# Kernel tuning notes

Hardware: AMD Instinct MI355X
Metric: run time of the kernel (lower is better)

The kernel has to match this reference:

```python
import jax, jax.numpy as jnp
import numpy as np

LRELU_SLOPE = 0.2
ACT_GAIN = float(np.sqrt(2.0))  # def_gain of lrelu in StyleGAN2
CLAMP = 256.0


def _affine(w, W, b):
    # StyleGAN2 FullyConnectedLayer: runtime weight gain 1/sqrt(in_features)
    return w @ W.T * (1.0 / np.sqrt(W.shape[1])) + b[None, :]


def _gather(x, fn, pad):
    # zero rows for padding faces appended at the end, then neighborhood gather
    padded = jnp.concatenate([x, jnp.zeros((pad, x.shape[1]), x.dtype)], axis=0)
    return padded[fn]  # [N, K, C]


def _mod_texture_conv(g, styles, wc, wsd, wcr):
    # g: [N, 9, I] gathered neighborhoods; styles: [B, I]
    B, I = styles.shape
    N = g.shape[0]
    F = N // B
    # position-typed 1x1 weights: [self, 4 sides, 4 corners] -> [O, I, 9]
    W = jnp.concatenate([wc[:, :, None],
                         jnp.repeat(wsd[:, :, None], 4, axis=2),
                         jnp.repeat(wcr[:, :, None], 4, axis=2)], axis=2)
    wmod = W[None] * styles[:, None, :, None]                    # [B,O,I,9] modulate
    d = jax.lax.rsqrt(jnp.sum(wmod * wmod, axis=(2, 3)) + 1e-8)  # [B,O] demodulate
    wmod = wmod * d[:, :, None, None]
    out = jnp.einsum('bfki,boik->bfok', g.reshape(B, F, 9, I), wmod)
    return out.max(axis=3).reshape(N, -1)  # MaxPool2d((1,9)) aggregation


def _smooth_upsample(x, pool_map, fn, pad):
    # replicate coarse face features to fine faces, then smooth over 9-neighborhood
    return _gather(x[pool_map], fn, pad).mean(axis=1)


def _act(x, bias):
    # clamp_gain(lrelu(x+b), act_gain*gain, 256*gain) with gain=1
    return jnp.clip(jax.nn.leaky_relu(x + bias[None, :], LRELU_SLOPE) * ACT_GAIN, -CLAMP, CLAMP)


def setup_inputs() -> dict:
    key = jax.random.key(0)
    ks = iter(jax.random.split(key, 40))
    B, Fc, Ff = 1, 32768, 131072
    IN, OUT, GEO, COL, WD = 128, 128, 32, 3, 512
    OC1 = OUT - GEO  # 96
    PAD0, PAD1 = 1024, 4096
    nk = lambda *s: jax.random.normal(next(ks), s, jnp.float32)
    ri = lambda shape, hi: jax.random.randint(next(ks), shape, 0, hi, jnp.int32).astype(jnp.int64)
    return dict(
        x=nk(B * Fc, IN - GEO), shape_feat=nk(B * Fc, GEO), img=nk(B * Fc, COL),
        ws=nk(B, 3, WD),
        fn0=ri((B * Fc, 9), B * Fc + PAD0), fn1=ri((B * Ff, 9), B * Ff + PAD1),
        pool_map0=ri((B * Ff,), B * Fc),
        pad0=PAD0, pad1=PAD1,
        affine0_w=nk(IN, WD), affine0_b=jnp.ones((IN,), jnp.float32),
        w_center0=nk(OUT, IN), w_side0=nk(OUT, IN), w_corner0=nk(OUT, IN),
        noise_strength0=nk(1) * 0.1, bias0=nk(OUT) * 0.1, noise_const0=nk(Ff),
        affine1_w=nk(OUT, WD), affine1_b=jnp.ones((OUT,), jnp.float32),
        w_center1=nk(OC1, OUT), w_side1=nk(OC1, OUT), w_corner1=nk(OC1, OUT),
        noise_strength1=nk(1) * 0.1, bias1=nk(OC1) * 0.1, noise_const1=nk(Ff),
        affine2_w=nk(OC1, WD), affine2_b=jnp.ones((OC1,), jnp.float32),
        w_rgb=nk(COL, OC1), bias_rgb=nk(COL) * 0.1,
    )


def reference(x, shape_feat, img, ws, fn0, fn1, pool_map0, pad0, pad1,
              affine0_w, affine0_b, w_center0, w_side0, w_corner0,
              noise_strength0, bias0, noise_const0,
              affine1_w, affine1_b, w_center1, w_side1, w_corner1,
              noise_strength1, bias1, noise_const1,
              affine2_w, affine2_b, w_rgb, bias_rgb):
    B = ws.shape[0]
    h = jnp.concatenate([x, shape_feat], axis=1)  # [B*Fc, IN]
    # ---- conv0: coarse-level modulated face conv, then SmoothUpsample to fine ----
    s0 = _affine(ws[:, 0], affine0_w, affine0_b)
    h = _mod_texture_conv(_gather(h, fn0, pad0), s0, w_center0, w_side0, w_corner0)
    h = _smooth_upsample(h, pool_map0, fn1, pad1)  # [B*Ff, OUT]
    h = h + jnp.tile(noise_const0[None, :], (B, 1)).reshape(-1, 1) * noise_strength0
    h = _act(h, bias0)
    # ---- conv1: fine-level modulated face conv ----
    s1 = _affine(ws[:, 1], affine1_w, affine1_b)
    h = _mod_texture_conv(_gather(h, fn1, pad1), s1, w_center1, w_side1, w_corner1)
    h = h + jnp.tile(noise_const1[None, :], (B, 1)).reshape(-1, 1) * noise_strength1
    h = _act(h, bias1)  # [B*Ff, 96]
    # ---- torgb: 1x1 modulated conv (demodulate=False), weight_gain on styles ----
    s2 = _affine(ws[:, 2], affine2_w, affine2_b) * (1.0 / np.sqrt(w_rgb.shape[1]))
    xg = _gather(h, fn1[:, :1], pad1)[:, 0]  # kernel_size^2 == 1 -> self gather
    y = jnp.einsum('bfi,oi,bi->bfo', xg.reshape(B, -1, xg.shape[1]), w_rgb, s2)
    y = jnp.clip(y.reshape(xg.shape[0], -1) + bias_rgb[None, :], -CLAMP, CLAMP)
    img_out = _smooth_upsample(img, pool_map0, fn1, pad1) + y
    return h, img_out
```

## Files before the change

kernel.cpp:

```cpp
#include <hip/hip_runtime.h>

#define FC 32768
#define FF 131072
#define LRELU_SLOPE 0.2f
#define ACT_GAIN 1.4142135623730951f
#define CLAMP_V 256.0f

typedef __bf16 bf16x8 __attribute__((ext_vector_type(8)));
typedef float f32x4 __attribute__((ext_vector_type(4)));
typedef float f32x2 __attribute__((ext_vector_type(2)));
typedef unsigned u32x4 __attribute__((ext_vector_type(4)));
typedef unsigned u32x2 __attribute__((ext_vector_type(2)));
typedef unsigned short u16x4 __attribute__((ext_vector_type(4)));

static __device__ __forceinline__ unsigned short f2bf(float f) {
    unsigned u = __float_as_uint(f);
    u += 0x7FFFu + ((u >> 16) & 1u);
    return (unsigned short)(u >> 16);
}
static __device__ __forceinline__ unsigned packbf(float a, float b) {
    return (unsigned)f2bf(a) | ((unsigned)f2bf(b) << 16);
}
static __device__ __forceinline__ float bf2f(unsigned short u) {
    return __uint_as_float(((unsigned)u) << 16);
}
static __device__ __forceinline__ float actf(float v) {
    v = (v < 0.f) ? v * LRELU_SLOPE : v;
    v *= ACT_GAIN;
    return fminf(fmaxf(v, -CLAMP_V), CLAMP_V);
}
static __device__ __forceinline__ int xcd_swz(int bid, int nwg) {
    return (bid & 7) * (nwg >> 3) + (bid >> 3);
}

__global__ void k_prep2(const float* __restrict__ wsvec,
                        const float* __restrict__ a0w, const float* __restrict__ a0b,
                        const float* __restrict__ a1w, const float* __restrict__ a1b,
                        const float* __restrict__ a2w, const float* __restrict__ a2b,
                        float* __restrict__ s0, float* __restrict__ s1, float* __restrict__ s2,
                        unsigned* __restrict__ zrow)
{
    int lane = threadIdx.x & 63;
    int t = blockIdx.x * 4 + (threadIdx.x >> 6);
    if (t >= 352) {
        if (t == 352) zrow[lane] = 0u;
        return;
    }
    int level, o;
    const float *W, *bptr; float* out;
    if (t < 128)       { level = 0; o = t;       W = a0w; bptr = a0b; out = s0; }
    else if (t < 256)  { level = 1; o = t - 128; W = a1w; bptr = a1b; out = s1; }
    else               { level = 2; o = t - 256; W = a2w; bptr = a2b; out = s2; }
    const float* wrow = wsvec + level * 512;
    const float* Wr = W + (size_t)o * 512;
    f32x4 wa = *(const f32x4*)(wrow + lane * 8);
    f32x4 wb = *(const f32x4*)(wrow + lane * 8 + 4);
    f32x4 va = *(const f32x4*)(Wr + lane * 8);
    f32x4 vb = *(const f32x4*)(Wr + lane * 8 + 4);
    float acc = wa.x * va.x + wa.y * va.y + wa.z * va.z + wa.w * va.w
              + wb.x * vb.x + wb.y * vb.y + wb.z * vb.z + wb.w * vb.w;
    #pragma unroll
    for (int off = 32; off; off >>= 1) acc += __shfl_down(acc, off, 64);
    if (lane == 0) {
        float v = acc * 0.04419417382415922f + bptr[o];
        if (level == 2) v *= 0.10206207261596577f;
        out[o] = v;
    }
}

__global__ void k_misc(const float* __restrict__ x, const float* __restrict__ sf,
                       u16x4* __restrict__ xcat,
                       const int* __restrict__ fn1, const int* __restrict__ pmap,
                       int* __restrict__ cidx)
{
    int b = blockIdx.x;
    if (b < FC * 32 / 256) {
        int gid = b * 256 + threadIdx.x;
        int f = gid >> 5;
        int c4 = (gid & 31) * 4;
        f32x4 v;
        if (c4 < 96) v = *(const f32x4*)(x + (size_t)f * 96 + c4);
        else         v = *(const f32x4*)(sf + (size_t)f * 32 + (c4 - 96));
        u16x4 o;
        o.x = f2bf(v.x); o.y = f2bf(v.y); o.z = f2bf(v.z); o.w = f2bf(v.w);
        xcat[gid] = o;
    } else {
        int gid = (b - FC * 32 / 256) * 256 + threadIdx.x;
        int g = fn1[gid];
        cidx[gid] = ((unsigned)g < FF) ? pmap[g] : -1;
    }
}

__global__ void k_wmod(const float* __restrict__ wc0, const float* __restrict__ wsd0,
                       const float* __restrict__ wcr0, const float* __restrict__ s0,
                       unsigned short* __restrict__ wm0,
                       const float* __restrict__ wc1, const float* __restrict__ wsd1,
                       const float* __restrict__ wcr1, const float* __restrict__ s1,
                       unsigned short* __restrict__ wm1,
                       const float* __restrict__ wrgb, const float* __restrict__ s2,
                       float* __restrict__ wrgbmod)
{
    int b = blockIdx.x;
    int i = threadIdx.x;
    if (b == 224) {
        for (int t = i; t < 288; t += 128) {
            int c = t / 96, k = t % 96;
            wrgbmod[c * 96 + k] = wrgb[c * 96 + k] * s2[k];
        }
        return;
    }
    const float *wc, *wsd, *wcr, *s; unsigned short* out; int o, O;
    if (b < 128) { wc = wc0; wsd = wsd0; wcr = wcr0; s = s0; out = wm0; o = b; O = 128; }
    else         { wc = wc1; wsd = wsd1; wcr = wcr1; s = s1; out = wm1; o = b - 128; O = 96; }
    float sv = s[i];
    float pc = wc[o * 128 + i] * sv;
    float ps = wsd[o * 128 + i] * sv;
    float pr = wcr[o * 128 + i] * sv;
    float part = pc * pc + 4.f * ps * ps + 4.f * pr * pr;
    __shared__ float red[2];
    #pragma unroll
    for (int off = 32; off; off >>= 1) part += __shfl_down(part, off, 64);
    if ((threadIdx.x & 63) == 0) red[threadIdx.x >> 6] = part;
    __syncthreads();
    float d = rsqrtf(red[0] + red[1] + 1e-8f);
    out[(0 * O + o) * 128 + i] = f2bf(pc * d);
    out[(1 * O + o) * 128 + i] = f2bf(ps * d);
    out[(2 * O + o) * 128 + i] = f2bf(pr * d);
}

__launch_bounds__(256, 2)
__global__ void k_fgemm0(const unsigned short* __restrict__ xcat,
                         const unsigned short* __restrict__ wm,
                         const int* __restrict__ fn0,
                         const unsigned* __restrict__ zrow,
                         unsigned* __restrict__ hc0)
{
    __shared__ char ldsw[65536];
    int bid = xcd_swz(blockIdx.x, gridDim.x);
    int lane = threadIdx.x & 63;
    int w = threadIdx.x >> 6;
    int fgrp = w >> 1;
    int mtb = (w & 1) * 4;
    int fbase = (bid * 2 + fgrp) * 16;
    int quad = lane >> 4, l15 = lane & 15;
    int face = fbase + l15;
    const char* hb = (const char*)xcat;
    const char* wb = (const char*)wm;

    #pragma unroll
    for (int i0 = 0; i0 < 16; ++i0) {
        int i = i0 * 256 + threadIdx.x;
        u32x4 v = *(const u32x4*)(wb + 32768 + (size_t)i * 16);
        int r = i >> 4, c = i & 15;
        *(u32x4*)(ldsw + r * 256 + ((c ^ (r & 7)) * 16)) = v;
    }
    __syncthreads();

    int id[9];
    #pragma unroll
    for (int j = 0; j < 9; ++j) id[j] = fn0[(size_t)face * 9 + j];

    f32x4 ymax[4];
    #pragma unroll
    for (int mi = 0; mi < 4; ++mi)
        #pragma unroll
        for (int r = 0; r < 4; ++r) ymax[mi][r] = -3.0e38f;

    int xr = l15 & 7;

    #pragma unroll
    for (int j = 0; j < 9; ++j) {
        const int t = (j == 0) ? 0 : ((j < 5) ? 1 : 2);
        const char* src = ((unsigned)id[j] < FC) ? (hb + (size_t)id[j] * 256) : (const char*)zrow;
        bf16x8 bfr[4];
        #pragma unroll
        for (int s = 0; s < 4; ++s)
            bfr[s] = *(const bf16x8*)(src + s * 64 + quad * 16);
        f32x4 acc[4];
        #pragma unroll
        for (int mi = 0; mi < 4; ++mi)
            #pragma unroll
            for (int r = 0; r < 4; ++r) acc[mi][r] = 0.f;
        #pragma unroll
        for (int s = 0; s < 4; ++s) {
            #pragma unroll
            for (int mi = 0; mi < 4; ++mi) {
                bf16x8 afr;
                if (t == 0)
                    afr = *(const bf16x8*)(wb + (size_t)((((mtb + mi) * 16 + l15) * 128 + s * 32 + quad * 8) * 2));
                else
                    afr = *(const bf16x8*)(ldsw + ((t - 1) * 128 + (mtb + mi) * 16 + l15) * 256
                                                + (((s * 4 + quad) ^ xr) * 16));
                acc[mi] = __builtin_amdgcn_mfma_f32_16x16x32_bf16(afr, bfr[s], acc[mi], 0, 0, 0);
            }
        }
        #pragma unroll
        for (int mi = 0; mi < 4; ++mi)
            #pragma unroll
            for (int r = 0; r < 4; ++r)
                ymax[mi][r] = fmaxf(ymax[mi][r], acc[mi][r]);
    }

    #pragma unroll
    for (int mi = 0; mi < 4; ++mi) {
        u32x2 v;
        v.x = packbf(ymax[mi][0], ymax[mi][1]);
        v.y = packbf(ymax[mi][2], ymax[mi][3]);
        *(u32x2*)(hc0 + (size_t)face * 64 + (mtb + mi) * 8 + quad * 2) = v;
    }
}

__global__ void k_upsample(const unsigned* __restrict__ hc, const int* __restrict__ cidx,
                           const float* __restrict__ nco0,
                           const float* __restrict__ ns0p, const float* __restrict__ bias0,
                           unsigned* __restrict__ h1u, const unsigned* __restrict__ zrow)
{
    int bid = xcd_swz(blockIdx.x, gridDim.x);
    int gid = bid * 256 + threadIdx.x;
    int f = gid >> 4;
    int c = gid & 15;
    int id[9];
    #pragma unroll
    for (int j = 0; j < 9; ++j) id[j] = cidx[f * 9 + j];
    u32x4 v[9];
    #pragma unroll
    for (int j = 0; j < 9; ++j) {
        const unsigned* p = (id[j] >= 0) ? (hc + (size_t)id[j] * 64) : zrow;
        v[j] = *(const u32x4*)(p + c * 4);
    }
    float nz = nco0[f] * ns0p[0];
    f32x4 b0 = *(const f32x4*)(bias0 + c * 8);
    f32x4 b1 = *(const f32x4*)(bias0 + c * 8 + 4);
    const float inv9 = 1.f / 9.f;
    u32x4 out;
    #pragma unroll
    for (int k = 0; k < 4; ++k) {
        float a0 = 0.f, a1 = 0.f;
        #pragma unroll
        for (int j = 0; j < 9; ++j) {
            a0 += bf2f((unsigned short)v[j][k]);
            a1 += bf2f((unsigned short)(v[j][k] >> 16));
        }
        float bb0 = (k < 2) ? ((k == 0) ? b0.x : b0.z) : ((k == 2) ? b1.x : b1.z);
        float bb1 = (k < 2) ? ((k == 0) ? b0.y : b0.w) : ((k == 2) ? b1.y : b1.w);
        a0 = actf(a0 * inv9 + nz + bb0);
        a1 = actf(a1 * inv9 + nz + bb1);
        out[k] = packbf(a0, a1);
    }
    *(u32x4*)(h1u + (size_t)f * 64 + c * 4) = out;
}

__launch_bounds__(256, 2)
__global__ void k_fgemm1(const unsigned short* __restrict__ h1,
                         const unsigned short* __restrict__ wm,
                         const int* __restrict__ fn1,
                         const unsigned* __restrict__ zrow,
                         const float* __restrict__ nco1, const float* __restrict__ ns1p,
                         const float* __restrict__ bias1, const float* __restrict__ wrgbmod,
                         float* __restrict__ hout, f32x4* __restrict__ rgb3)
{
    __shared__ char ldsw[49152];
    int bid = xcd_swz(blockIdx.x, gridDim.x);
    int lane = threadIdx.x & 63;
    int w = threadIdx.x >> 6;
    int fbase = (bid * 4 + w) * 16;
    int quad = lane >> 4, l15 = lane & 15;
    int face = fbase + l15;
    const char* hb = (const char*)h1;
    const char* wb = (const char*)wm;

    #pragma unroll
    for (int i0 = 0; i0 < 12; ++i0) {
        int i = i0 * 256 + threadIdx.x;
        u32x4 v = *(const u32x4*)(wb + 24576 + (size_t)i * 16);
        int r = i >> 4, c = i & 15;
        *(u32x4*)(ldsw + r * 256 + ((c ^ (r & 7)) * 16)) = v;
    }
    __syncthreads();

    int id[9];
    #pragma unroll
    for (int j = 0; j < 9; ++j) id[j] = fn1[(size_t)face * 9 + j];

    f32x4 ymax[6];
    #pragma unroll
    for (int mt = 0; mt < 6; ++mt)
        #pragma unroll
        for (int r = 0; r < 4; ++r) ymax[mt][r] = -3.0e38f;

    int xr = l15 & 7;

    #pragma unroll
    for (int j = 0; j < 9; ++j) {
        const int t = (j == 0) ? 0 : ((j < 5) ? 1 : 2);
        const char* src = ((unsigned)id[j] < FF) ? (hb + (size_t)id[j] * 256) : (const char*)zrow;
        bf16x8 bfr[4];
        #pragma unroll
        for (int s = 0; s < 4; ++s)
            bfr[s] = *(const bf16x8*)(src + s * 64 + quad * 16);
        f32x4 acc[6];
        #pragma unroll
        for (int mt = 0; mt < 6; ++mt)
            #pragma unroll
            for (int r = 0; r < 4; ++r) acc[mt][r] = 0.f;
        #pragma unroll
        for (int s = 0; s < 4; ++s) {
            #pragma unroll
            for (int mt = 0; mt < 6; ++mt) {
                bf16x8 afr;
                if (t == 0)
                    afr = *(const bf16x8*)(wb + (size_t)(((mt * 16 + l15) * 128 + s * 32 + quad * 8) * 2));
                else
                    afr = *(const bf16x8*)(ldsw + ((t - 1) * 96 + mt * 16 + l15) * 256
                                                + (((s * 4 + quad) ^ xr) * 16));
                acc[mt] = __builtin_amdgcn_mfma_f32_16x16x32_bf16(afr, bfr[s], acc[mt], 0, 0, 0);
            }
        }
        #pragma unroll
        for (int mt = 0; mt < 6; ++mt)
            #pragma unroll
            for (int r = 0; r < 4; ++r)
                ymax[mt][r] = fmaxf(ymax[mt][r], acc[mt][r]);
    }

    float ns1 = ns1p[0];
    float nz = nco1[face] * ns1;
    float p0 = 0.f, p1 = 0.f, p2 = 0.f;
    #pragma unroll
    for (int mt = 0; mt < 6; ++mt) {
        f32x4 bv = *(const f32x4*)(bias1 + mt * 16 + quad * 4);
        f32x4 hv;
        #pragma unroll
        for (int r = 0; r < 4; ++r) hv[r] = actf(ymax[mt][r] + nz + bv[r]);
        __builtin_nontemporal_store(hv, (f32x4*)(hout + (size_t)face * 96 + mt * 16 + quad * 4));
        f32x4 w0 = *(const f32x4*)(wrgbmod + mt * 16 + quad * 4);
        f32x4 w1 = *(const f32x4*)(wrgbmod + 96 + mt * 16 + quad * 4);
        f32x4 w2 = *(const f32x4*)(wrgbmod + 192 + mt * 16 + quad * 4);
        p0 += hv.x * w0.x + hv.y * w0.y + hv.z * w0.z + hv.w * w0.w;
        p1 += hv.x * w1.x + hv.y * w1.y + hv.z * w1.z + hv.w * w1.w;
        p2 += hv.x * w2.x + hv.y * w2.y + hv.z * w2.z + hv.w * w2.w;
    }
    p0 += __shfl_xor(p0, 16, 64); p0 += __shfl_xor(p0, 32, 64);
    p1 += __shfl_xor(p1, 16, 64); p1 += __shfl_xor(p1, 32, 64);
    p2 += __shfl_xor(p2, 16, 64); p2 += __shfl_xor(p2, 32, 64);
    if (quad == 0) {
        f32x4 o; o.x = p0; o.y = p1; o.z = p2; o.w = 0.f;
        rgb3[face] = o;
    }
}

__global__ void k_torgb2(const f32x4* __restrict__ rgb3, const int* __restrict__ fn1,
                         const int* __restrict__ cidx, const float* __restrict__ img,
                         const float* __restrict__ brgb, float* __restrict__ imgout)
{
    int f = blockIdx.x * 256 + threadIdx.x;
    int g0 = fn1[(size_t)f * 9];
    float y0 = 0.f, y1 = 0.f, y2 = 0.f;
    if ((unsigned)g0 < FF) {
        f32x4 y = rgb3[g0];
        y0 = y.x; y1 = y.y; y2 = y.z;
    }
    y0 = fminf(fmaxf(y0 + brgb[0], -CLAMP_V), CLAMP_V);
    y1 = fminf(fmaxf(y1 + brgb[1], -CLAMP_V), CLAMP_V);
    y2 = fminf(fmaxf(y2 + brgb[2], -CLAMP_V), CLAMP_V);
    float i0 = 0.f, i1 = 0.f, i2 = 0.f;
    #pragma unroll
    for (int j = 0; j < 9; ++j) {
        int id = cidx[f * 9 + j];
        if (id >= 0) {
            const float* ir = img + (size_t)id * 3;
            i0 += ir[0]; i1 += ir[1]; i2 += ir[2];
        }
    }
    const float inv9 = 1.f / 9.f;
    imgout[(size_t)f * 3 + 0] = i0 * inv9 + y0;
    imgout[(size_t)f * 3 + 1] = i1 * inv9 + y1;
    imgout[(size_t)f * 3 + 2] = i2 * inv9 + y2;
}

extern "C" void kernel_launch(void* const* d_in, const int* in_sizes, int n_in,
                              void* d_out, int out_size, void* d_ws, size_t ws_size,
                              hipStream_t stream) {
    const float* x     = (const float*)d_in[0];
    const float* sfeat = (const float*)d_in[1];
    const float* img   = (const float*)d_in[2];
    const float* wsv   = (const float*)d_in[3];
    const int* fn0     = (const int*)d_in[4];
    const int* fn1     = (const int*)d_in[5];
    const int* pmap    = (const int*)d_in[6];
    const float* a0w   = (const float*)d_in[9];
    const float* a0b   = (const float*)d_in[10];
    const float* wc0   = (const float*)d_in[11];
    const float* wsd0  = (const float*)d_in[12];
    const float* wcr0  = (const float*)d_in[13];
    const float* ns0   = (const float*)d_in[14];
    const float* bias0 = (const float*)d_in[15];
    const float* nco0  = (const float*)d_in[16];
    const float* a1w   = (const float*)d_in[17];
    const float* a1b   = (const float*)d_in[18];
    const float* wc1   = (const float*)d_in[19];
    const float* wsd1  = (const float*)d_in[20];
    const float* wcr1  = (const float*)d_in[21];
    const float* ns1   = (const float*)d_in[22];
    const float* bias1 = (const float*)d_in[23];
    const float* nco1  = (const float*)d_in[24];
    const float* a2w   = (const float*)d_in[25];
    const float* a2b   = (const float*)d_in[26];
    const float* wrgb  = (const float*)d_in[27];
    const float* brgb  = (const float*)d_in[28];

    char* wsb = (char*)d_ws;
    float* s0            = (float*)(wsb + 0);
    float* s1            = (float*)(wsb + 512);
    float* s2            = (float*)(wsb + 1024);
    float* wrgbmod       = (float*)(wsb + 1536);
    unsigned* zrow       = (unsigned*)(wsb + 4096);
    unsigned short* wm0  = (unsigned short*)(wsb + 8192);
    unsigned short* wm1  = (unsigned short*)(wsb + 8192 + 98304);
    unsigned short* xcat = (unsigned short*)(wsb + 262144);
    unsigned* hc0        = (unsigned*)(wsb + 33816576);
    unsigned short* h1   = (unsigned short*)(wsb + 42205184);
    int* cidx            = (int*)(wsb + 75759616);
    f32x4* rgb3          = (f32x4*)(wsb + 155975680);

    float* out_h   = (float*)d_out;
    float* out_img = out_h + (size_t)FF * 96;

    k_misc<<<FC * 32 / 256 + FF * 9 / 256, 256, 0, stream>>>(x, sfeat, (u16x4*)xcat, fn1, pmap, cidx);
    k_prep2<<<89, 256, 0, stream>>>(wsv, a0w, a0b, a1w, a1b, a2w, a2b, s0, s1, s2, zrow);
    k_wmod<<<225, 128, 0, stream>>>(wc0, wsd0, wcr0, s0, wm0,
                                    wc1, wsd1, wcr1, s1, wm1, wrgb, s2, wrgbmod);
    k_fgemm0<<<FC / 32, 256, 0, stream>>>(xcat, wm0, fn0, zrow, hc0);
    k_upsample<<<FF * 16 / 256, 256, 0, stream>>>(hc0, cidx, nco0, ns0, bias0, (unsigned*)h1, zrow);
    k_fgemm1<<<FF / 64, 256, 0, stream>>>(h1, wm1, fn1, zrow, nco1, ns1, bias1, wrgbmod,
                                          out_h, rgb3);
    k_torgb2<<<FF / 256, 256, 0, stream>>>(rgb3, fn1, cidx, img, brgb, out_img);
}
```

Measured before the change: 287.6 us.

## Double-buffer neighbor gathers and split fgemm1 output channels across wave pairs

```diff
diff --git a/kernel.cpp b/kernel.cpp
--- a/kernel.cpp
+++ b/kernel.cpp
@@ -8,7 +8,6 @@
 
 typedef __bf16 bf16x8 __attribute__((ext_vector_type(8)));
 typedef float f32x4 __attribute__((ext_vector_type(4)));
-typedef float f32x2 __attribute__((ext_vector_type(2)));
 typedef unsigned u32x4 __attribute__((ext_vector_type(4)));
 typedef unsigned u32x2 __attribute__((ext_vector_type(2)));
 typedef unsigned short u16x4 __attribute__((ext_vector_type(4)));
@@ -168,14 +167,25 @@
 
     int xr = l15 & 7;
 
-    #pragma unroll
-    for (int j = 0; j < 9; ++j) {
-        const int t = (j == 0) ? 0 : ((j < 5) ? 1 : 2);
-        const char* src = ((unsigned)id[j] < FC) ? (hb + (size_t)id[j] * 256) : (const char*)zrow;
-        bf16x8 bfr[4];
-        #pragma unroll
-        for (int s = 0; s < 4; ++s)
-            bfr[s] = *(const bf16x8*)(src + s * 64 + quad * 16);
+    bf16x8 b0[4], b1[4];
+    {
+        const char* src = ((unsigned)id[1] < FC) ? (hb + (size_t)id[1] * 256) : (const char*)zrow;
+        #pragma unroll
+        for (int s = 0; s < 4; ++s) b0[s] = *(const bf16x8*)(src + s * 64 + quad * 16);
+    }
+
+    #pragma unroll
+    for (int jj = 1; jj <= 8; ++jj) {
+        const int t = (jj < 5) ? 1 : 2;
+        const int nj = (jj < 8) ? (jj + 1) : 0;
+        {
+            const char* src = ((unsigned)id[nj] < FC) ? (hb + (size_t)id[nj] * 256) : (const char*)zrow;
+            #pragma unroll
+            for (int s = 0; s < 4; ++s) {
+                bf16x8 v = *(const bf16x8*)(src + s * 64 + quad * 16);
+                if (jj & 1) b1[s] = v; else b0[s] = v;
+            }
+        }
         f32x4 acc[4];
         #pragma unroll
         for (int mi = 0; mi < 4; ++mi)
@@ -183,15 +193,33 @@
             for (int r = 0; r < 4; ++r) acc[mi][r] = 0.f;
         #pragma unroll
         for (int s = 0; s < 4; ++s) {
+            bf16x8 cur = (jj & 1) ? b0[s] : b1[s];
             #pragma unroll
             for (int mi = 0; mi < 4; ++mi) {
-                bf16x8 afr;
-                if (t == 0)
-                    afr = *(const bf16x8*)(wb + (size_t)((((mtb + mi) * 16 + l15) * 128 + s * 32 + quad * 8) * 2));
-                else
-                    afr = *(const bf16x8*)(ldsw + ((t - 1) * 128 + (mtb + mi) * 16 + l15) * 256
-                                                + (((s * 4 + quad) ^ xr) * 16));
-                acc[mi] = __builtin_amdgcn_mfma_f32_16x16x32_bf16(afr, bfr[s], acc[mi], 0, 0, 0);
+                bf16x8 afr = *(const bf16x8*)(ldsw + ((t - 1) * 128 + (mtb + mi) * 16 + l15) * 256
+                                                   + (((s * 4 + quad) ^ xr) * 16));
+                acc[mi] = __builtin_amdgcn_mfma_f32_16x16x32_bf16(afr, cur, acc[mi], 0, 0, 0);
+            }
+        }
+        #pragma unroll
+        for (int mi = 0; mi < 4; ++mi)
+            #pragma unroll
+            for (int r = 0; r < 4; ++r)
+                ymax[mi][r] = fmaxf(ymax[mi][r], acc[mi][r]);
+    }
+
+    {
+        f32x4 acc[4];
+        #pragma unroll
+        for (int mi = 0; mi < 4; ++mi)
+            #pragma unroll
+            for (int r = 0; r < 4; ++r) acc[mi][r] = 0.f;
+        #pragma unroll
+        for (int s = 0; s < 4; ++s) {
+            #pragma unroll
+            for (int mi = 0; mi < 4; ++mi) {
+                bf16x8 afr = *(const bf16x8*)(wb + (size_t)((((mtb + mi) * 16 + l15) * 128 + s * 32 + quad * 8) * 2));
+                acc[mi] = __builtin_amdgcn_mfma_f32_16x16x32_bf16(afr, b0[s], acc[mi], 0, 0, 0);
             }
         }
         #pragma unroll
@@ -260,10 +288,14 @@
                          float* __restrict__ hout, f32x4* __restrict__ rgb3)
 {
     __shared__ char ldsw[49152];
+    __shared__ float rgx[2][16][4];
     int bid = xcd_swz(blockIdx.x, gridDim.x);
     int lane = threadIdx.x & 63;
     int w = threadIdx.x >> 6;
-    int fbase = (bid * 4 + w) * 16;
+    int fgrp = w >> 1;
+    int chh = w & 1;
+    int mtb = chh * 3;
+    int fbase = (bid * 2 + fgrp) * 16;
     int quad = lane >> 4, l15 = lane & 15;
     int face = fbase + l15;
     const char* hb = (const char*)h1;
@@ -282,56 +314,86 @@
     #pragma unroll
     for (int j = 0; j < 9; ++j) id[j] = fn1[(size_t)face * 9 + j];
 
-    f32x4 ymax[6];
-    #pragma unroll
-    for (int mt = 0; mt < 6; ++mt)
-        #pragma unroll
-        for (int r = 0; r < 4; ++r) ymax[mt][r] = -3.0e38f;
+    f32x4 ymax[3];
+    #pragma unroll
+    for (int k = 0; k < 3; ++k)
+        #pragma unroll
+        for (int r = 0; r < 4; ++r) ymax[k][r] = -3.0e38f;
 
     int xr = l15 & 7;
 
-    #pragma unroll
-    for (int j = 0; j < 9; ++j) {
-        const int t = (j == 0) ? 0 : ((j < 5) ? 1 : 2);
-        const char* src = ((unsigned)id[j] < FF) ? (hb + (size_t)id[j] * 256) : (const char*)zrow;
-        bf16x8 bfr[4];
-        #pragma unroll
-        for (int s = 0; s < 4; ++s)
-            bfr[s] = *(const bf16x8*)(src + s * 64 + quad * 16);
-        f32x4 acc[6];
-        #pragma unroll
-        for (int mt = 0; mt < 6; ++mt)
-            #pragma unroll
-            for (int r = 0; r < 4; ++r) acc[mt][r] = 0.f;
+    bf16x8 b0[4], b1[4];
+    {
+        const char* src = ((unsigned)id[1] < FF) ? (hb + (size_t)id[1] * 256) : (const char*)zrow;
+        #pragma unroll
+        for (int s = 0; s < 4; ++s) b0[s] = *(const bf16x8*)(src + s * 64 + quad * 16);
+    }
+
+    #pragma unroll
+    for (int jj = 1; jj <= 8; ++jj) {
+        const int t = (jj < 5) ? 1 : 2;
+        const int nj = (jj < 8) ? (jj + 1) : 0;
+        {
+            const char* src = ((unsigned)id[nj] < FF) ? (hb + (size_t)id[nj] * 256) : (const char*)zrow;
+            #pragma unroll
+            for (int s = 0; s < 4; ++s) {
+                bf16x8 v = *(const bf16x8*)(src + s * 64 + quad * 16);
+                if (jj & 1) b1[s] = v; else b0[s] = v;
+            }
+        }
+        f32x4 acc[3];
+        #pragma unroll
+        for (int k = 0; k < 3; ++k)
+            #pragma unroll
+            for (int r = 0; r < 4; ++r) acc[k][r] = 0.f;
         #pragma unroll
         for (int s = 0; s < 4; ++s) {
-            #pragma unroll
-            for (int mt = 0; mt < 6; ++mt) {
-                bf16x8 afr;
-                if (t == 0)
-                    afr = *(const bf16x8*)(wb + (size_t)(((mt * 16 + l15) * 128 + s * 32 + quad * 8) * 2));
-                else
-                    afr = *(const bf16x8*)(ldsw + ((t - 1) * 96 + mt * 16 + l15) * 256
-                                                + (((s * 4 + quad) ^ xr) * 16));
-                acc[mt] = __builtin_amdgcn_mfma_f32_16x16x32_bf16(afr, bfr[s], acc[mt], 0, 0, 0);
+            bf16x8 cur = (jj & 1) ? b0[s] : b1[s];
+            #pragma unroll
+            for (int k = 0; k < 3; ++k) {
+                bf16x8 afr = *(const bf16x8*)(ldsw + ((t - 1) * 96 + (mtb + k) * 16 + l15) * 256
+                                                   + (((s * 4 + quad) ^ xr) * 16));
+                acc[k] = __builtin_amdgcn_mfma_f32_16x16x32_bf16(afr, cur, acc[k], 0, 0, 0);
             }
         }
         #pragma unroll
-        for (int mt = 0; mt < 6; ++mt)
+        for (int k = 0; k < 3; ++k)
             #pragma unroll
             for (int r = 0; r < 4; ++r)
-                ymax[mt][r] = fmaxf(ymax[mt][r], acc[mt][r]);
+                ymax[k][r] = fmaxf(ymax[k][r], acc[k][r]);
+    }
+
+    {
+        f32x4 acc[3];
+        #pragma unroll
+        for (int k = 0; k < 3; ++k)
+            #pragma unroll
+            for (int r = 0; r < 4; ++r) acc[k][r] = 0.f;
+        #pragma unroll
+        for (int s = 0; s < 4; ++s) {
+            #pragma unroll
+            for (int k = 0; k < 3; ++k) {
+                bf16x8 afr = *(const bf16x8*)(wb + (size_t)((((mtb + k) * 16 + l15) * 128 + s * 32 + quad * 8) * 2));
+                acc[k] = __builtin_amdgcn_mfma_f32_16x16x32_bf16(afr, b0[s], acc[k], 0, 0, 0);
+            }
+        }
+        #pragma unroll
+        for (int k = 0; k < 3; ++k)
+            #pragma unroll
+            for (int r = 0; r < 4; ++r)
+                ymax[k][r] = fmaxf(ymax[k][r], acc[k][r]);
     }
 
     float ns1 = ns1p[0];
     float nz = nco1[face] * ns1;
     float p0 = 0.f, p1 = 0.f, p2 = 0.f;
     #pragma unroll
-    for (int mt = 0; mt < 6; ++mt) {
+    for (int k = 0; k < 3; ++k) {
+        int mt = mtb + k;
         f32x4 bv = *(const f32x4*)(bias1 + mt * 16 + quad * 4);
         f32x4 hv;
         #pragma unroll
-        for (int r = 0; r < 4; ++r) hv[r] = actf(ymax[mt][r] + nz + bv[r]);
+        for (int r = 0; r < 4; ++r) hv[r] = actf(ymax[k][r] + nz + bv[r]);
         __builtin_nontemporal_store(hv, (f32x4*)(hout + (size_t)face * 96 + mt * 16 + quad * 4));
         f32x4 w0 = *(const f32x4*)(wrgbmod + mt * 16 + quad * 4);
         f32x4 w1 = *(const f32x4*)(wrgbmod + 96 + mt * 16 + quad * 4);
@@ -343,8 +405,16 @@
     p0 += __shfl_xor(p0, 16, 64); p0 += __shfl_xor(p0, 32, 64);
     p1 += __shfl_xor(p1, 16, 64); p1 += __shfl_xor(p1, 32, 64);
     p2 += __shfl_xor(p2, 16, 64); p2 += __shfl_xor(p2, 32, 64);
-    if (quad == 0) {
-        f32x4 o; o.x = p0; o.y = p1; o.z = p2; o.w = 0.f;
+    if (chh == 1 && quad == 0) {
+        rgx[fgrp][l15][0] = p0; rgx[fgrp][l15][1] = p1; rgx[fgrp][l15][2] = p2;
+    }
+    __syncthreads();
+    if (chh == 0 && quad == 0) {
+        f32x4 o;
+        o.x = p0 + rgx[fgrp][l15][0];
+        o.y = p1 + rgx[fgrp][l15][1];
+        o.z = p2 + rgx[fgrp][l15][2];
+        o.w = 0.f;
         rgb3[face] = o;
     }
 }
@@ -432,7 +502,7 @@
                                     wc1, wsd1, wcr1, s1, wm1, wrgb, s2, wrgbmod);
     k_fgemm0<<<FC / 32, 256, 0, stream>>>(xcat, wm0, fn0, zrow, hc0);
     k_upsample<<<FF * 16 / 256, 256, 0, stream>>>(hc0, cidx, nco0, ns0, bias0, (unsigned*)h1, zrow);
-    k_fgemm1<<<FF / 64, 256, 0, stream>>>(h1, wm1, fn1, zrow, nco1, ns1, bias1, wrgbmod,
+    k_fgemm1<<<FF / 32, 256, 0, stream>>>(h1, wm1, fn1, zrow, nco1, ns1, bias1, wrgbmod,
                                           out_h, rgb3);
     k_torgb2<<<FF / 256, 256, 0, stream>>>(rgb3, fn1, cidx, img, brgb, out_img);
 }
```

After: 313.8 us. +9.1%, slower.
